# Performance work log

Hardware: AMD Instinct MI355X
Metric: run time of the kernel (lower is better)

Reference implementation:

```python
import jax, jax.numpy as jnp
import numpy as np

SCALE = 0.08838834764831845  # 1/sqrt(head_dim=128)


def setup_inputs() -> dict:
    key = jax.random.key(0)
    ks = jax.random.split(key, 5)
    B, H, D = 16, 8, 128          # batch (decode seqs), kv heads, head_dim
    BS, BPS = 16, 128             # block_size, blocks per sequence
    NBLK = B * BPS                # total cache blocks (2048)
    CTX = 2048                    # context length per sequence
    q = jax.random.normal(ks[0], (B, H, D), jnp.float32)
    k = jax.random.normal(ks[1], (B, H, D), jnp.float32)
    v = jax.random.normal(ks[2], (B, H, D), jnp.float32)
    k_cache = jax.random.normal(ks[3], (NBLK, BS, H, D), jnp.float32)
    v_cache = jax.random.normal(ks[4], (NBLK, BS, H, D), jnp.float32)
    # each sequence owns a distinct contiguous set of blocks
    block_tables = jnp.arange(B * BPS, dtype=jnp.int32).reshape(B, BPS)
    context_lens = jnp.full((B,), CTX, dtype=jnp.int32)
    # slot for the newest token (position CTX-1) of each sequence
    last = CTX - 1
    slot_mapping = block_tables[:, last // BS] * BS + (last % BS)
    return {"q": q, "k": k, "v": v, "k_cache": k_cache, "v_cache": v_cache,
            "slot_mapping": slot_mapping.astype(jnp.int32),
            "block_tables": block_tables, "context_lens": context_lens}


def reference(q, k, v, k_cache, v_cache, slot_mapping, block_tables, context_lens):
    # ---- store_kvcache: scatter new k/v tokens into paged caches ----
    nblk, bs, H, D = k_cache.shape
    k_cache = k_cache.reshape(nblk * bs, H, D).at[slot_mapping].set(k).reshape(nblk, bs, H, D)
    v_cache = v_cache.reshape(nblk * bs, H, D).at[slot_mapping].set(v).reshape(nblk, bs, H, D)

    # ---- _sdpa_decode: paged gather + masked attention (q_per_seq = 1) ----
    B, nb = block_tables.shape
    T = nb * bs                              # max tokens per sequence
    token_idx = jnp.arange(T, dtype=jnp.int32)
    block_idx = token_idx // bs
    token_off = token_idx % bs
    block_ids = block_tables[:, block_idx]   # [B, T]
    k_all = k_cache[block_ids, token_off]    # [B, T, H, D]
    v_all = v_cache[block_ids, token_off]    # [B, T, H, D]

    valid = token_idx[None, :] < context_lens[:, None]           # [B, T]
    q_pos = context_lens - 1                                     # q_per_seq == 1
    causal = token_idx[None, :] <= q_pos[:, None]                # [B, T]
    mask = valid & causal

    scores = jnp.einsum("bhd,bthd->bht", q, k_all) * SCALE       # [B, H, T]
    scores = jnp.where(mask[:, None, :], scores, -jnp.inf)
    p = jax.nn.softmax(scores, axis=-1)
    out = jnp.einsum("bht,bthd->bhd", p, v_all)                  # [B, H, D]
    return out
```

## Files before the change

kernel.cpp:

```cpp
#include <hip/hip_runtime.h>
#include <math.h>

#define B_ 16
#define H_ 8
#define D_ 128
#define BS_ 16
#define BPS_ 128
#define T_ (BPS_ * BS_)
#define ROW_ (H_ * D_)
#define SCALE_ 0.08838834764831845f

template<int NS>
__global__ __launch_bounds__(256, 4) void attn_partial(
    const float* __restrict__ q,
    const float* __restrict__ knew,
    const float* __restrict__ vnew,
    const float* __restrict__ kc,
    const float* __restrict__ vc,
    const int* __restrict__ btab,
    const int* __restrict__ clen,
    float* __restrict__ ws_m,
    float* __restrict__ ws_l,
    float* __restrict__ ws_o)
{
    constexpr int CHUNK = T_ / NS;
    constexpr int TPW = CHUNK / 4;
    constexpr int NBLK_C = CHUNK / BS_;

    const int cix = blockIdx.x;
    const int b = blockIdx.y;
    const int tid = threadIdx.x;
    const int wave = tid >> 6;
    const int lane = tid & 63;
    const int hl = lane & 31;
    const int half = lane >> 5;
    const int ctx = clen[b];
    const int cs = cix * CHUNK;
    const int t0 = wave * TPW;

    __shared__ int   s_bt[NBLK_C];
    __shared__ float s_m[4][H_], s_l[4][H_], s_c[4][H_];
    __shared__ float s_oacc[4][H_][D_];

    if (tid < NBLK_C) s_bt[tid] = btab[b * BPS_ + cix * NBLK_C + tid];

    float4 q4[4];
    #pragma unroll
    for (int j = 0; j < 4; ++j)
        q4[j] = *(const float4*)(q + (size_t)b * ROW_ + j * 256 + half * 128 + 4 * hl);
    __syncthreads();

    float m[4], l[4];
    float4 acc[4];
    #pragma unroll
    for (int j = 0; j < 4; ++j) {
        m[j] = -1e30f;
        l[j] = 0.f;
        acc[j] = make_float4(0.f, 0.f, 0.f, 0.f);
    }

    auto load_tok = [&](int t, float4 (&kd)[4], float4 (&vd)[4]) {
        const int tg = cs + t0 + t;
        const int blk = s_bt[(t0 + t) >> 4];
        const float* krb = (tg == ctx - 1)
            ? (knew + (size_t)b * ROW_)
            : (kc + ((size_t)blk * BS_ + (tg & 15)) * ROW_);
        const float* vrb = (tg == ctx - 1)
            ? (vnew + (size_t)b * ROW_)
            : (vc + ((size_t)blk * BS_ + (tg & 15)) * ROW_);
        #pragma unroll
        for (int j = 0; j < 4; ++j) {
            kd[j] = *(const float4*)(krb + j * 256 + half * 128 + 4 * hl);
            vd[j] = *(const float4*)(vrb + j * 256 + half * 128 + 4 * hl);
        }
    };

    auto compute = [&](int t, float4 (&kd)[4], float4 (&vd)[4]) {
        const int tg = cs + t0 + t;
        float s[4];
        #pragma unroll
        for (int j = 0; j < 4; ++j) {
            float ss = q4[j].x * kd[j].x + q4[j].y * kd[j].y
                     + q4[j].z * kd[j].z + q4[j].w * kd[j].w;
            ss += __shfl_xor(ss, 16);
            ss += __shfl_xor(ss, 8);
            ss += __shfl_xor(ss, 4);
            ss += __shfl_xor(ss, 2);
            ss += __shfl_xor(ss, 1);
            s[j] = (tg < ctx) ? ss * SCALE_ : -INFINITY;
        }
        #pragma unroll
        for (int j = 0; j < 4; ++j) {
            const float mn = fmaxf(m[j], s[j]);
            const float al = __expf(m[j] - mn);
            const float p  = __expf(s[j] - mn);
            m[j] = mn;
            l[j] = l[j] * al + p;
            acc[j].x = acc[j].x * al + p * vd[j].x;
            acc[j].y = acc[j].y * al + p * vd[j].y;
            acc[j].z = acc[j].z * al + p * vd[j].z;
            acc[j].w = acc[j].w * al + p * vd[j].w;
        }
    };

    float4 kA[4], vA[4], kB[4], vB[4];
    load_tok(0, kA, vA);
    #pragma unroll
    for (int tt = 0; tt < TPW / 2; ++tt) {
        load_tok(2 * tt + 1, kB, vB);
        compute(2 * tt, kA, vA);
        if (2 * tt + 2 < TPW) load_tok(2 * tt + 2, kA, vA);
        compute(2 * tt + 1, kB, vB);
    }

    #pragma unroll
    for (int j = 0; j < 4; ++j) {
        *(float4*)&s_oacc[wave][2 * j + half][4 * hl] = acc[j];
        if (hl == 0) {
            s_m[wave][2 * j + half] = m[j];
            s_l[wave][2 * j + half] = l[j];
        }
    }
    __syncthreads();

    if (tid < H_) {
        const int h = tid;
        float M = fmaxf(fmaxf(s_m[0][h], s_m[1][h]), fmaxf(s_m[2][h], s_m[3][h]));
        float L = 0.f;
        #pragma unroll
        for (int w = 0; w < 4; ++w) {
            const float cf = __expf(s_m[w][h] - M);
            s_c[w][h] = cf;
            L += s_l[w][h] * cf;
        }
        const int idx = (b * H_ + h) * NS + cix;
        ws_m[idx] = M;
        ws_l[idx] = L;
    }
    __syncthreads();
    for (int r = tid; r < H_ * D_; r += 256) {
        const int h = r >> 7, d = r & 127;
        const float oo = s_oacc[0][h][d] * s_c[0][h] + s_oacc[1][h][d] * s_c[1][h]
                       + s_oacc[2][h][d] * s_c[2][h] + s_oacc[3][h][d] * s_c[3][h];
        ws_o[((size_t)(b * H_ + h) * NS + cix) * D_ + d] = oo;
    }
}

template<int NS>
__global__ __launch_bounds__(128) void attn_reduce(
    const float* __restrict__ ws_m,
    const float* __restrict__ ws_l,
    const float* __restrict__ ws_o,
    float* __restrict__ out)
{
    const int bh = blockIdx.x;
    const int tid = threadIdx.x;

    __shared__ float s_co[NS];
    __shared__ float s_lg;

    if (tid < 64) {
        float m = -INFINITY;
        for (int cc = tid; cc < NS; cc += 64) m = fmaxf(m, ws_m[bh * NS + cc]);
        m = fmaxf(m, __shfl_xor(m, 32));
        m = fmaxf(m, __shfl_xor(m, 16));
        m = fmaxf(m, __shfl_xor(m, 8));
        m = fmaxf(m, __shfl_xor(m, 4));
        m = fmaxf(m, __shfl_xor(m, 2));
        m = fmaxf(m, __shfl_xor(m, 1));
        float lw = 0.f;
        for (int cc = tid; cc < NS; cc += 64) {
            const float co = __expf(ws_m[bh * NS + cc] - m);
            s_co[cc] = co;
            lw += ws_l[bh * NS + cc] * co;
        }
        lw += __shfl_xor(lw, 32);
        lw += __shfl_xor(lw, 16);
        lw += __shfl_xor(lw, 8);
        lw += __shfl_xor(lw, 4);
        lw += __shfl_xor(lw, 2);
        lw += __shfl_xor(lw, 1);
        if (tid == 0) s_lg = lw;
    }
    __syncthreads();

    float acc = 0.f;
    #pragma unroll 8
    for (int cc = 0; cc < NS; ++cc)
        acc += s_co[cc] * ws_o[((size_t)bh * NS + cc) * D_ + tid];
    out[(size_t)bh * D_ + tid] = acc / s_lg;
}

template<int NS>
static void launch_all(const float* q, const float* knew, const float* vnew,
                       const float* kc, const float* vc,
                       const int* btab, const int* clen,
                       float* ws, float* out, hipStream_t stream)
{
    float* ws_m = ws;
    float* ws_l = ws + B_ * H_ * NS;
    float* ws_o = ws + 2 * B_ * H_ * NS;
    attn_partial<NS><<<dim3(NS, B_), 256, 0, stream>>>(q, knew, vnew, kc, vc,
                                                       btab, clen, ws_m, ws_l, ws_o);
    attn_reduce<NS><<<dim3(B_ * H_), 128, 0, stream>>>(ws_m, ws_l, ws_o, out);
}

extern "C" void kernel_launch(void* const* d_in, const int* in_sizes, int n_in,
                              void* d_out, int out_size, void* d_ws, size_t ws_size,
                              hipStream_t stream) {
    const float* q    = (const float*)d_in[0];
    const float* knew = (const float*)d_in[1];
    const float* vnew = (const float*)d_in[2];
    const float* kc   = (const float*)d_in[3];
    const float* vc   = (const float*)d_in[4];
    const int* btab = (const int*)d_in[6];
    const int* clen = (const int*)d_in[7];
    float* out = (float*)d_out;
    float* ws  = (float*)d_ws;

    const size_t need64 = (size_t)B_ * H_ * 64 * (2 + D_) * sizeof(float);
    const size_t need32 = (size_t)B_ * H_ * 32 * (2 + D_) * sizeof(float);
    if (ws_size >= need64)      launch_all<64>(q, knew, vnew, kc, vc, btab, clen, ws, out, stream);
    else if (ws_size >= need32) launch_all<32>(q, knew, vnew, kc, vc, btab, clen, ws, out, stream);
    else                        launch_all<16>(q, knew, vnew, kc, vc, btab, clen, ws, out, stream);
}
```

Before: 315.2 us.

## Stage K/V tokens through LDS with async global_load_lds double buffering

Replaces the register-prefetch loop with direct global-to-LDS DMA (global_load_lds) into a double-buffered shared tile, where each wave handles one token per tile and the block synchronises after every tile. Block-table entries move into registers, and the output accumulation buffer now reuses the staging memory. The aim is to overlap memory fetches with compute and cut VGPR pressure. In exchange it uses 64KB of LDS per block, adds a __syncthreads per token step, interleaves tokens across waves, and lowers the occupancy hint to 2. Nothing explicitly waits for the async LDS loads to complete before they are read, so correctness depends on what the compiler inserts.

```diff
diff --git a/kernel.cpp b/kernel.cpp
--- a/kernel.cpp
+++ b/kernel.cpp
@@ -10,8 +10,15 @@
 #define ROW_ (H_ * D_)
 #define SCALE_ 0.08838834764831845f
 
+__device__ __forceinline__ void dma16(const float* g, float* l) {
+    __builtin_amdgcn_global_load_lds(
+        (__attribute__((address_space(1))) void*)g,
+        (__attribute__((address_space(3))) void*)l,
+        16, 0, 0);
+}
+
 template<int NS>
-__global__ __launch_bounds__(256, 4) void attn_partial(
+__global__ __launch_bounds__(256, 2) void attn_partial(
     const float* __restrict__ q,
     const float* __restrict__ knew,
     const float* __restrict__ vnew,
@@ -24,7 +31,7 @@
     float* __restrict__ ws_o)
 {
     constexpr int CHUNK = T_ / NS;
-    constexpr int TPW = CHUNK / 4;
+    constexpr int NTILES = CHUNK / 4;
     constexpr int NBLK_C = CHUNK / BS_;
 
     const int cix = blockIdx.x;
@@ -36,19 +43,18 @@
     const int half = lane >> 5;
     const int ctx = clen[b];
     const int cs = cix * CHUNK;
-    const int t0 = wave * TPW;
-
-    __shared__ int   s_bt[NBLK_C];
+
+    __shared__ float smem[2][4][2][ROW_];
     __shared__ float s_m[4][H_], s_l[4][H_], s_c[4][H_];
-    __shared__ float s_oacc[4][H_][D_];
-
-    if (tid < NBLK_C) s_bt[tid] = btab[b * BPS_ + cix * NBLK_C + tid];
+
+    int bt[NBLK_C];
+    #pragma unroll
+    for (int i = 0; i < NBLK_C; ++i) bt[i] = btab[b * BPS_ + cs / BS_ + i];
 
     float4 q4[4];
     #pragma unroll
     for (int j = 0; j < 4; ++j)
         q4[j] = *(const float4*)(q + (size_t)b * ROW_ + j * 256 + half * 128 + 4 * hl);
-    __syncthreads();
 
     float m[4], l[4];
     float4 acc[4];
@@ -59,60 +65,69 @@
         acc[j] = make_float4(0.f, 0.f, 0.f, 0.f);
     }
 
-    auto load_tok = [&](int t, float4 (&kd)[4], float4 (&vd)[4]) {
-        const int tg = cs + t0 + t;
-        const int blk = s_bt[(t0 + t) >> 4];
-        const float* krb = (tg == ctx - 1)
-            ? (knew + (size_t)b * ROW_)
-            : (kc + ((size_t)blk * BS_ + (tg & 15)) * ROW_);
-        const float* vrb = (tg == ctx - 1)
-            ? (vnew + (size_t)b * ROW_)
-            : (vc + ((size_t)blk * BS_ + (tg & 15)) * ROW_);
-        #pragma unroll
-        for (int j = 0; j < 4; ++j) {
-            kd[j] = *(const float4*)(krb + j * 256 + half * 128 + 4 * hl);
-            vd[j] = *(const float4*)(vrb + j * 256 + half * 128 + 4 * hl);
-        }
-    };
-
-    auto compute = [&](int t, float4 (&kd)[4], float4 (&vd)[4]) {
-        const int tg = cs + t0 + t;
-        float s[4];
-        #pragma unroll
-        for (int j = 0; j < 4; ++j) {
-            float ss = q4[j].x * kd[j].x + q4[j].y * kd[j].y
-                     + q4[j].z * kd[j].z + q4[j].w * kd[j].w;
-            ss += __shfl_xor(ss, 16);
-            ss += __shfl_xor(ss, 8);
-            ss += __shfl_xor(ss, 4);
-            ss += __shfl_xor(ss, 2);
-            ss += __shfl_xor(ss, 1);
-            s[j] = (tg < ctx) ? ss * SCALE_ : -INFINITY;
-        }
-        #pragma unroll
-        for (int j = 0; j < 4; ++j) {
-            const float mn = fmaxf(m[j], s[j]);
-            const float al = __expf(m[j] - mn);
-            const float p  = __expf(s[j] - mn);
-            m[j] = mn;
-            l[j] = l[j] * al + p;
-            acc[j].x = acc[j].x * al + p * vd[j].x;
-            acc[j].y = acc[j].y * al + p * vd[j].y;
-            acc[j].z = acc[j].z * al + p * vd[j].z;
-            acc[j].w = acc[j].w * al + p * vd[j].w;
-        }
-    };
-
-    float4 kA[4], vA[4], kB[4], vB[4];
-    load_tok(0, kA, vA);
-    #pragma unroll
-    for (int tt = 0; tt < TPW / 2; ++tt) {
-        load_tok(2 * tt + 1, kB, vB);
-        compute(2 * tt, kA, vA);
-        if (2 * tt + 2 < TPW) load_tok(2 * tt + 2, kA, vA);
-        compute(2 * tt + 1, kB, vB);
-    }
-
+    #define STAGE(buf, tile_c, blkid)                                           \
+    {                                                                           \
+        const int t_ = (tile_c) * 4 + wave;                                     \
+        const int tg_ = cs + t_;                                                \
+        const float* krb_ = (tg_ == ctx - 1)                                    \
+            ? (knew + (size_t)b * ROW_)                                         \
+            : (kc + ((size_t)(blkid) * BS_ + (tg_ & 15)) * ROW_);               \
+        const float* vrb_ = (tg_ == ctx - 1)                                    \
+            ? (vnew + (size_t)b * ROW_)                                         \
+            : (vc + ((size_t)(blkid) * BS_ + (tg_ & 15)) * ROW_);               \
+        _Pragma("unroll")                                                       \
+        for (int qq = 0; qq < 4; ++qq) {                                        \
+            dma16(krb_ + qq * 256 + lane * 4, &smem[buf][wave][0][qq * 256]);   \
+            dma16(vrb_ + qq * 256 + lane * 4, &smem[buf][wave][1][qq * 256]);   \
+        }                                                                       \
+    }
+
+    STAGE(0, 0, bt[0]);
+    __syncthreads();
+
+    #pragma unroll
+    for (int tile = 0; tile < NTILES; ++tile) {
+        if (tile + 1 < NTILES) STAGE((tile + 1) & 1, tile + 1, bt[(tile + 1) >> 2]);
+
+        {
+            const int t = tile * 4 + wave;
+            const int tg = cs + t;
+            float4 kd[4], vd[4];
+            #pragma unroll
+            for (int j = 0; j < 4; ++j) {
+                kd[j] = *(const float4*)&smem[tile & 1][wave][0][j * 256 + half * 128 + 4 * hl];
+                vd[j] = *(const float4*)&smem[tile & 1][wave][1][j * 256 + half * 128 + 4 * hl];
+            }
+            float s[4];
+            #pragma unroll
+            for (int j = 0; j < 4; ++j) {
+                float ss = q4[j].x * kd[j].x + q4[j].y * kd[j].y
+                         + q4[j].z * kd[j].z + q4[j].w * kd[j].w;
+                ss += __shfl_xor(ss, 16);
+                ss += __shfl_xor(ss, 8);
+                ss += __shfl_xor(ss, 4);
+                ss += __shfl_xor(ss, 2);
+                ss += __shfl_xor(ss, 1);
+                s[j] = (tg < ctx) ? ss * SCALE_ : -INFINITY;
+            }
+            #pragma unroll
+            for (int j = 0; j < 4; ++j) {
+                const float mn = fmaxf(m[j], s[j]);
+                const float al = __expf(m[j] - mn);
+                const float p  = __expf(s[j] - mn);
+                m[j] = mn;
+                l[j] = l[j] * al + p;
+                acc[j].x = acc[j].x * al + p * vd[j].x;
+                acc[j].y = acc[j].y * al + p * vd[j].y;
+                acc[j].z = acc[j].z * al + p * vd[j].z;
+                acc[j].w = acc[j].w * al + p * vd[j].w;
+            }
+        }
+        __syncthreads();
+    }
+    #undef STAGE
+
+    float (*s_oacc)[H_][D_] = reinterpret_cast<float(*)[H_][D_]>(&smem[0][0][0][0]);
     #pragma unroll
     for (int j = 0; j < 4; ++j) {
         *(float4*)&s_oacc[wave][2 * j + half][4 * hl] = acc[j];
```

Result: faster. 297.7 us (-5.5%).
